# Kernel tuning notes

Hardware: AMD Instinct MI355X
Metric: run time of the kernel (lower is better)

Reference implementation:

```python
import jax, jax.numpy as jnp
import numpy as np

N_NODES = 100000
N_EDGES = 3200000
N_GRAPHS = 1024


def _glorot(key, shape):
    fan_in, fan_out = shape[0], shape[1]
    lim = jnp.sqrt(6.0 / (fan_in + fan_out))
    return jax.random.uniform(key, shape, minval=-lim, maxval=lim, dtype=jnp.float32)


def setup_inputs() -> dict:
    key = jax.random.key(0)
    ks = jax.random.split(key, 9)
    x = jax.random.normal(ks[0], (N_NODES, 3), dtype=jnp.float32)
    edge_index = jax.random.randint(ks[1], (2, N_EDGES), 0, N_NODES, dtype=jnp.int64)
    batch = jnp.sort(jax.random.randint(ks[2], (N_NODES,), 0, N_GRAPHS, dtype=jnp.int64))
    return {
        "x": x,
        "edge_index": edge_index,
        "batch": batch,
        "W1": _glorot(ks[3], (3, 16)),
        "b1": jnp.zeros((16,), jnp.float32),
        "W2": _glorot(ks[4], (16, 16)),
        "b2": jnp.zeros((16,), jnp.float32),
        "Wl": _glorot(ks[5], (16, 7)),
        "bl": jnp.zeros((7,), jnp.float32),
    }


def gcn_conv(x, edge_index, W, b, num_nodes):
    """GCNConv with normalize=True, add_self_loops=True (PyG defaults)."""
    x = x @ W  # linear transform first: [N, F_out]
    loop = jnp.arange(num_nodes, dtype=edge_index.dtype)
    row = jnp.concatenate([edge_index[0], loop])  # source nodes
    col = jnp.concatenate([edge_index[1], loop])  # target nodes
    # degree of target nodes (edge weight 1 incl. self loops)
    deg = jax.ops.segment_sum(jnp.ones_like(col, dtype=x.dtype), col,
                              num_segments=num_nodes)
    dinv = jnp.where(deg > 0, jax.lax.rsqrt(deg), 0.0)
    norm = dinv[row] * dinv[col]  # [E+N]
    msg = x[row] * norm[:, None]  # gather + normalize
    out = jax.ops.segment_sum(msg, col, num_segments=num_nodes)  # scatter-add
    return out + b


def reference(x, edge_index, batch, W1, b1, W2, b2, Wl, bl):
    h = jax.nn.relu(gcn_conv(x, edge_index, W1, b1, N_NODES))
    h = gcn_conv(h, edge_index, W2, b2, N_NODES)
    pooled = jax.ops.segment_sum(h, batch, num_segments=N_GRAPHS)  # global_add_pool
    logits = pooled @ Wl + bl  # [G, 7]
    return jax.nn.log_softmax(logits, axis=1)
```

## Files before the change

kernel.cpp:

```cpp
#include <hip/hip_runtime.h>
#include <hip/hip_fp16.h>
#include <math.h>

#define N_NODES  100000
#define N_EDGES  3200000
#define N_GRAPHS 1024
#define NBUCK    782
#define CAP      4608
#define NPS      500
#define ECH      6400

__device__ inline unsigned pack2(float a, float b) {
    union { __half2 h; unsigned u; } c;
    c.h = __floats2half2_rn(a, b);
    return c.u;
}
__device__ inline float2 up2(unsigned u) {
    union { unsigned u; __half2 h; } c; c.u = u;
    return __half22float2(c.h);
}
__device__ inline void acc8(float* a, uint4 v) {
    float2 f;
    f = up2(v.x); a[0] += f.x; a[1] += f.y;
    f = up2(v.y); a[2] += f.x; a[3] += f.y;
    f = up2(v.z); a[4] += f.x; a[5] += f.y;
    f = up2(v.w); a[6] += f.x; a[7] += f.y;
}
__device__ inline void acc4(float* a, uint2 v) {
    float2 f;
    f = up2(v.x); a[0] += f.x; a[1] += f.y;
    f = up2(v.y); a[2] += f.x; a[3] += f.y;
}

__global__ void k_pair_scatter(const int* __restrict__ row, const int* __restrict__ col,
                               int* __restrict__ gcursor, int* __restrict__ pairbuf) {
    __shared__ int            sbuf[ECH];
    __shared__ unsigned short sbk[ECH];
    __shared__ int            lhist[NBUCK];
    __shared__ int            lcur[NBUCK];
    int t = threadIdx.x;
    int e0 = blockIdx.x * ECH;
    const int4* col4 = (const int4*)(col + e0);
    const int4* row4 = (const int4*)(row + e0);
    for (int j = t; j < NBUCK; j += 256) lhist[j] = 0;
    __syncthreads();
    for (int k = t; k < ECH / 4; k += 256) {
        int4 c = col4[k];
        atomicAdd(&lhist[c.x >> 7], 1);
        atomicAdd(&lhist[c.y >> 7], 1);
        atomicAdd(&lhist[c.z >> 7], 1);
        atomicAdd(&lhist[c.w >> 7], 1);
    }
    __syncthreads();
    if (t < 64) {
        int carry = 0;
        for (int c0 = 0; c0 < NBUCK; c0 += 64) {
            int idx = c0 + t;
            int v = (idx < NBUCK) ? lhist[idx] : 0;
            int orig = v;
#pragma unroll
            for (int o = 1; o < 64; o <<= 1) {
                int u = __shfl_up(v, o, 64);
                if (t >= o) v += u;
            }
            if (idx < NBUCK) lcur[idx] = v - orig + carry;
            carry += __shfl(v, 63, 64);
        }
    }
    __syncthreads();
    for (int j = t; j < NBUCK; j += 256) {
        int c = lhist[j];
        int g = c ? atomicAdd(&gcursor[j], c) : 0;
        lhist[j] = j * CAP + g - lcur[j];
    }
    __syncthreads();
    for (int k = t; k < ECH / 4; k += 256) {
        int4 c = col4[k];
        int4 r = row4[k];
        int bk, pos;
        bk = c.x >> 7; pos = atomicAdd(&lcur[bk], 1);
        sbuf[pos] = r.x | ((c.x & 127) << 17); sbk[pos] = (unsigned short)bk;
        bk = c.y >> 7; pos = atomicAdd(&lcur[bk], 1);
        sbuf[pos] = r.y | ((c.y & 127) << 17); sbk[pos] = (unsigned short)bk;
        bk = c.z >> 7; pos = atomicAdd(&lcur[bk], 1);
        sbuf[pos] = r.z | ((c.z & 127) << 17); sbk[pos] = (unsigned short)bk;
        bk = c.w >> 7; pos = atomicAdd(&lcur[bk], 1);
        sbuf[pos] = r.w | ((c.w & 127) << 17); sbk[pos] = (unsigned short)bk;
    }
    __syncthreads();
    for (int k4 = t; k4 < ECH / 4; k4 += 256) {
        int k = k4 << 2;
        int4 v = ((const int4*)sbuf)[k4];
        ushort4 bb = ((const ushort4*)sbk)[k4];
        int p0 = lhist[bb.x] + k;
        int p1 = lhist[bb.y] + k + 1;
        int p2 = lhist[bb.z] + k + 2;
        int p3 = lhist[bb.w] + k + 3;
        if (p0 < (bb.x + 1) * CAP) pairbuf[p0] = v.x;
        if (p1 < (bb.y + 1) * CAP) pairbuf[p1] = v.y;
        if (p2 < (bb.z + 1) * CAP) pairbuf[p2] = v.z;
        if (p3 < (bb.w + 1) * CAP) pairbuf[p3] = v.w;
    }
}

__global__ void k_finalize(int* __restrict__ pairbuf, const int* __restrict__ gcursor,
                           int2* __restrict__ rowse, float* __restrict__ dinv,
                           const float* __restrict__ x, const float* __restrict__ W1,
                           __half* __restrict__ bufA16) {
    __shared__ int slice[CAP];
    __shared__ int lcnt[128];
    __shared__ int ls[128];
    __shared__ int cur[128];
    __shared__ float sw1[48];
    int t = threadIdx.x, b = blockIdx.x;
    int base = b * CAP;
    int cnt_b = gcursor[b];
    if (cnt_b > CAP) cnt_b = CAP;
    int cnt4 = cnt_b >> 2;
    if (t < 128) lcnt[t] = 0;
    if (t < 48) sw1[t] = W1[t];
    {
        const int4* pb4 = (const int4*)(pairbuf + base);
        for (int k4 = t; k4 < cnt4; k4 += 256) ((int4*)slice)[k4] = pb4[k4];
        int k = (cnt4 << 2) + t;
        if (k < cnt_b) slice[k] = pairbuf[base + k];
    }
    __syncthreads();
    for (int k4 = t; k4 < cnt4; k4 += 256) {
        int4 v = ((const int4*)slice)[k4];
        atomicAdd(&lcnt[(v.x >> 17) & 127], 1);
        atomicAdd(&lcnt[(v.y >> 17) & 127], 1);
        atomicAdd(&lcnt[(v.z >> 17) & 127], 1);
        atomicAdd(&lcnt[(v.w >> 17) & 127], 1);
    }
    {
        int k = (cnt4 << 2) + t;
        if (k < cnt_b) atomicAdd(&lcnt[(slice[k] >> 17) & 127], 1);
    }
    __syncthreads();
    int myc = (t < 128) ? lcnt[t] : 0;
    if (t < 128) ls[t] = myc;
    __syncthreads();
    for (int o = 1; o < 128; o <<= 1) {
        int v = (t < 128 && t >= o) ? ls[t - o] : 0;
        __syncthreads();
        if (t < 128) ls[t] += v;
        __syncthreads();
    }
    int node = (b << 7) + t;
    if (t < 128) {
        int st = base + ls[t] - myc;
        cur[t] = st;
        if (node < N_NODES) {
            rowse[node] = make_int2(st, st + myc);
            float d = rsqrtf((float)(myc + 1));
            dinv[node] = d;
            float x0 = x[node * 3 + 0], x1 = x[node * 3 + 1], x2 = x[node * 3 + 2];
            float v[16];
#pragma unroll
            for (int j = 0; j < 16; j++)
                v[j] = (x0 * sw1[j] + x1 * sw1[16 + j] + x2 * sw1[32 + j]) * d;
            uint4 u0 = { pack2(v[0], v[1]), pack2(v[2], v[3]), pack2(v[4], v[5]), pack2(v[6], v[7]) };
            uint4 u1 = { pack2(v[8], v[9]), pack2(v[10], v[11]), pack2(v[12], v[13]), pack2(v[14], v[15]) };
            uint4* p = (uint4*)(bufA16 + (long long)node * 16);
            p[0] = u0; p[1] = u1;
        }
    }
    __syncthreads();
    for (int k4 = t; k4 < cnt4; k4 += 256) {
        int4 v = ((const int4*)slice)[k4];
        int pos;
        pos = atomicAdd(&cur[(v.x >> 17) & 127], 1); pairbuf[pos] = v.x & 0x1FFFF;
        pos = atomicAdd(&cur[(v.y >> 17) & 127], 1); pairbuf[pos] = v.y & 0x1FFFF;
        pos = atomicAdd(&cur[(v.z >> 17) & 127], 1); pairbuf[pos] = v.z & 0x1FFFF;
        pos = atomicAdd(&cur[(v.w >> 17) & 127], 1); pairbuf[pos] = v.w & 0x1FFFF;
    }
    {
        int k = (cnt4 << 2) + t;
        if (k < cnt_b) {
            int p = slice[k];
            int pos = atomicAdd(&cur[(p >> 17) & 127], 1);
            pairbuf[pos] = p & 0x1FFFF;
        }
    }
}

__global__ void k_gather1(const uint4* __restrict__ src16, const int* __restrict__ csr,
                          const int2* __restrict__ rowse, const float* __restrict__ dinv,
                          const float* __restrict__ b1, const float* __restrict__ W2,
                          __half* __restrict__ out16) {
    __shared__ float sh[64][17];
    __shared__ float sW[256];
    __shared__ float sb1[16];
    int t = threadIdx.x;
    sW[t] = W2[t]; sW[t + 128] = W2[t + 128];
    if (t < 16) sb1[t] = b1[t];
    int local = t >> 1, h = t & 1;
    int node = blockIdx.x * 64 + local;
    bool act = node < N_NODES;
    int2 se = act ? rowse[node] : make_int2(0, 0);
    int s = se.x, e = se.y;
    float acc[8] = {0, 0, 0, 0, 0, 0, 0, 0};
    if (act) {
        uint4 u = src16[node * 2 + h];
        float2 f;
        f = up2(u.x); acc[0] = f.x; acc[1] = f.y;
        f = up2(u.y); acc[2] = f.x; acc[3] = f.y;
        f = up2(u.z); acc[4] = f.x; acc[5] = f.y;
        f = up2(u.w); acc[6] = f.x; acc[7] = f.y;
    }
    int j = s;
    for (; j < e && (j & 3); j++) acc8(acc, src16[csr[j] * 2 + h]);
    for (; j + 8 <= e; j += 8) {
        int4 ia = *(const int4*)(csr + j);
        int4 ib = *(const int4*)(csr + j + 4);
        uint4 v0 = src16[ia.x * 2 + h], v1 = src16[ia.y * 2 + h];
        uint4 v2 = src16[ia.z * 2 + h], v3 = src16[ia.w * 2 + h];
        uint4 v4 = src16[ib.x * 2 + h], v5 = src16[ib.y * 2 + h];
        uint4 v6 = src16[ib.z * 2 + h], v7 = src16[ib.w * 2 + h];
        acc8(acc, v0); acc8(acc, v1); acc8(acc, v2); acc8(acc, v3);
        acc8(acc, v4); acc8(acc, v5); acc8(acc, v6); acc8(acc, v7);
    }
    for (; j < e; j++) acc8(acc, src16[csr[j] * 2 + h]);
    float d = act ? dinv[node] : 0.f;
#pragma unroll
    for (int k = 0; k < 8; k++) {
        float v = acc[k] * d + sb1[h * 8 + k];
        sh[local][h * 8 + k] = v > 0.f ? v : 0.f;
    }
    __syncthreads();
    float v[8];
#pragma unroll
    for (int jj = 0; jj < 8; jj++) {
        int jo = h * 8 + jj;
        float a = 0.f;
#pragma unroll
        for (int k = 0; k < 16; k++) a += sh[local][k] * sW[k * 16 + jo];
        v[jj] = a * d;
    }
    if (act) {
        uint4 u = { pack2(v[0], v[1]), pack2(v[2], v[3]), pack2(v[4], v[5]), pack2(v[6], v[7]) };
        ((uint4*)(out16 + (long long)node * 16 + h * 8))[0] = u;
    }
}

__global__ void k_gather2(const uint2* __restrict__ src16, const int* __restrict__ csr,
                          const int2* __restrict__ rowse, const float* __restrict__ dinv,
                          const int* __restrict__ batch, float* __restrict__ pooled) {
    __shared__ float pl[8][16];
    __shared__ int ginfo[2];
    int t = threadIdx.x;
    int node0 = blockIdx.x * 64;
    if (t < 128) pl[t >> 4][t & 15] = 0.f;
    if (t == 0) {
        int last = node0 + 63; if (last >= N_NODES) last = N_NODES - 1;
        ginfo[0] = batch[node0];
        ginfo[1] = batch[last];
    }
    __syncthreads();
    int node = node0 + (t >> 2);
    int h = t & 3;
    float o[4] = {0, 0, 0, 0};
    bool act = node < N_NODES;
    if (act) {
        int2 se = rowse[node];
        int s = se.x, e = se.y;
        uint2 u = src16[node * 4 + h];
        float2 f;
        f = up2(u.x); o[0] = f.x; o[1] = f.y;
        f = up2(u.y); o[2] = f.x; o[3] = f.y;
        int j = s;
        for (; j < e && (j & 3); j++) acc4(o, src16[csr[j] * 4 + h]);
        for (; j + 8 <= e; j += 8) {
            int4 ia = *(const int4*)(csr + j);
            int4 ib = *(const int4*)(csr + j + 4);
            uint2 v0 = src16[ia.x * 4 + h], v1 = src16[ia.y * 4 + h];
            uint2 v2 = src16[ia.z * 4 + h], v3 = src16[ia.w * 4 + h];
            uint2 v4 = src16[ib.x * 4 + h], v5 = src16[ib.y * 4 + h];
            uint2 v6 = src16[ib.z * 4 + h], v7 = src16[ib.w * 4 + h];
            acc4(o, v0); acc4(o, v1); acc4(o, v2); acc4(o, v3);
            acc4(o, v4); acc4(o, v5); acc4(o, v6); acc4(o, v7);
        }
        for (; j < e; j++) acc4(o, src16[csr[j] * 4 + h]);
        float d = dinv[node];
        o[0] *= d; o[1] *= d; o[2] *= d; o[3] *= d;
        int slot = batch[node] - ginfo[0];
        if (slot < 8) {
#pragma unroll
            for (int k = 0; k < 4; k++) atomicAdd(&pl[slot][h * 4 + k], o[k]);
        } else {
#pragma unroll
            for (int k = 0; k < 4; k++) atomicAdd(&pooled[batch[node] * 16 + h * 4 + k], o[k]);
        }
    }
    __syncthreads();
    if (t < 128) {
        int s = t >> 4, f = t & 15;
        int span = ginfo[1] - ginfo[0];
        if (s <= span && s < 8)
            atomicAdd(&pooled[(ginfo[0] + s) * 16 + f], pl[s][f]);
    }
}

__global__ void k_head(const float* __restrict__ pooled, const int* __restrict__ batch,
                       const float* __restrict__ b2, const float* __restrict__ Wl,
                       const float* __restrict__ bl, float* __restrict__ out) {
    int g = blockIdx.x;
    int t = threadIdx.x;
    __shared__ int range[2];
    __shared__ float pld[16];
    __shared__ float logits[7];
    if (t < 2) {
        int target = g + t;
        int lo = 0, hi = N_NODES;
        while (lo < hi) {
            int mid = (lo + hi) >> 1;
            if (batch[mid] < target) lo = mid + 1; else hi = mid;
        }
        range[t] = lo;
    }
    __syncthreads();
    float cnt = (float)(range[1] - range[0]);
    if (t < 16) pld[t] = pooled[g * 16 + t] + cnt * b2[t];
    __syncthreads();
    if (t < 7) {
        float a = bl[t];
#pragma unroll
        for (int k = 0; k < 16; k++) a += pld[k] * Wl[k * 7 + t];
        logits[t] = a;
    }
    __syncthreads();
    if (t == 0) {
        float m = logits[0];
#pragma unroll
        for (int c = 1; c < 7; c++) m = fmaxf(m, logits[c]);
        float sum = 0.f;
#pragma unroll
        for (int c = 0; c < 7; c++) sum += expf(logits[c] - m);
        float lse = logf(sum) + m;
#pragma unroll
        for (int c = 0; c < 7; c++) out[g * 7 + c] = logits[c] - lse;
    }
}

extern "C" void kernel_launch(void* const* d_in, const int* in_sizes, int n_in,
                              void* d_out, int out_size, void* d_ws, size_t ws_size,
                              hipStream_t stream) {
    const float* x     = (const float*)d_in[0];
    const int*   ei    = (const int*)d_in[1];
    const int*   batch = (const int*)d_in[2];
    const float* W1    = (const float*)d_in[3];
    const float* b1    = (const float*)d_in[4];
    const float* W2    = (const float*)d_in[5];
    const float* b2    = (const float*)d_in[6];
    const float* Wl    = (const float*)d_in[7];
    const float* bl    = (const float*)d_in[8];
    float* out = (float*)d_out;

    const int* row = ei;
    const int* col = ei + N_EDGES;

    int*    gcursor = (int*)d_ws;
    float*  pooled  = (float*)d_ws + 800;
    float*  dinv    = (float*)d_ws + 17200;
    int2*   rowse   = (int2*)((int*)d_ws + 117200);
    int*    pairbuf = (int*)d_ws + 317200;
    __half* bufA16  = (__half*)((int*)d_ws + 3920656);
    __half* bufB16  = (__half*)((int*)d_ws + 4720656);

    const int BT = 256;

    hipMemsetAsync(gcursor, 0, 17184 * sizeof(int), stream);
    k_pair_scatter<<<NPS, BT, 0, stream>>>(row, col, gcursor, pairbuf);
    k_finalize<<<NBUCK, BT, 0, stream>>>(pairbuf, gcursor, rowse, dinv, x, W1, bufA16);
    k_gather1<<<(N_NODES + 63) / 64, 128, 0, stream>>>((const uint4*)bufA16, pairbuf, rowse,
                                                       dinv, b1, W2, bufB16);
    k_gather2<<<(N_NODES + 63) / 64, BT, 0, stream>>>((const uint2*)bufB16, pairbuf, rowse,
                                                      dinv, batch, pooled);
    k_head<<<N_GRAPHS, 64, 0, stream>>>(pooled, batch, b2, Wl, bl, out);
}
```

Measured before the change: 201.3 us.

## Aggregate raw 3-dim inputs before W1 in first GCN layer

```diff
diff --git a/kernel.cpp b/kernel.cpp
--- a/kernel.cpp
+++ b/kernel.cpp
@@ -18,13 +18,6 @@
 __device__ inline float2 up2(unsigned u) {
     union { unsigned u; __half2 h; } c; c.u = u;
     return __half22float2(c.h);
-}
-__device__ inline void acc8(float* a, uint4 v) {
-    float2 f;
-    f = up2(v.x); a[0] += f.x; a[1] += f.y;
-    f = up2(v.y); a[2] += f.x; a[3] += f.y;
-    f = up2(v.z); a[4] += f.x; a[5] += f.y;
-    f = up2(v.w); a[6] += f.x; a[7] += f.y;
 }
 __device__ inline void acc4(float* a, uint2 v) {
     float2 f;
@@ -105,20 +98,17 @@
 
 __global__ void k_finalize(int* __restrict__ pairbuf, const int* __restrict__ gcursor,
                            int2* __restrict__ rowse, float* __restrict__ dinv,
-                           const float* __restrict__ x, const float* __restrict__ W1,
-                           __half* __restrict__ bufA16) {
+                           const float* __restrict__ x, __half* __restrict__ bufA16) {
     __shared__ int slice[CAP];
     __shared__ int lcnt[128];
     __shared__ int ls[128];
     __shared__ int cur[128];
-    __shared__ float sw1[48];
     int t = threadIdx.x, b = blockIdx.x;
     int base = b * CAP;
     int cnt_b = gcursor[b];
     if (cnt_b > CAP) cnt_b = CAP;
     int cnt4 = cnt_b >> 2;
     if (t < 128) lcnt[t] = 0;
-    if (t < 48) sw1[t] = W1[t];
     {
         const int4* pb4 = (const int4*)(pairbuf + base);
         for (int k4 = t; k4 < cnt4; k4 += 256) ((int4*)slice)[k4] = pb4[k4];
@@ -156,14 +146,8 @@
             float d = rsqrtf((float)(myc + 1));
             dinv[node] = d;
             float x0 = x[node * 3 + 0], x1 = x[node * 3 + 1], x2 = x[node * 3 + 2];
-            float v[16];
-#pragma unroll
-            for (int j = 0; j < 16; j++)
-                v[j] = (x0 * sw1[j] + x1 * sw1[16 + j] + x2 * sw1[32 + j]) * d;
-            uint4 u0 = { pack2(v[0], v[1]), pack2(v[2], v[3]), pack2(v[4], v[5]), pack2(v[6], v[7]) };
-            uint4 u1 = { pack2(v[8], v[9]), pack2(v[10], v[11]), pack2(v[12], v[13]), pack2(v[14], v[15]) };
-            uint4* p = (uint4*)(bufA16 + (long long)node * 16);
-            p[0] = u0; p[1] = u1;
+            uint2 u = { pack2(x0 * d, x1 * d), pack2(x2 * d, 0.f) };
+            ((uint2*)(bufA16 + (long long)node * 4))[0] = u;
         }
     }
     __syncthreads();
@@ -185,63 +169,60 @@
     }
 }
 
-__global__ void k_gather1(const uint4* __restrict__ src16, const int* __restrict__ csr,
+__global__ void k_gather1(const uint2* __restrict__ src16, const int* __restrict__ csr,
                           const int2* __restrict__ rowse, const float* __restrict__ dinv,
-                          const float* __restrict__ b1, const float* __restrict__ W2,
-                          __half* __restrict__ out16) {
-    __shared__ float sh[64][17];
-    __shared__ float sW[256];
+                          const float* __restrict__ W1, const float* __restrict__ b1,
+                          const float* __restrict__ W2, __half* __restrict__ out16) {
+    __shared__ float sW1[48];
     __shared__ float sb1[16];
+    __shared__ float sW2[256];
     int t = threadIdx.x;
-    sW[t] = W2[t]; sW[t + 128] = W2[t + 128];
+    sW2[t] = W2[t];
+    if (t < 48) sW1[t] = W1[t];
     if (t < 16) sb1[t] = b1[t];
-    int local = t >> 1, h = t & 1;
-    int node = blockIdx.x * 64 + local;
-    bool act = node < N_NODES;
-    int2 se = act ? rowse[node] : make_int2(0, 0);
+    __syncthreads();
+    int node = blockIdx.x * 256 + t;
+    if (node >= N_NODES) return;
+    int2 se = rowse[node];
     int s = se.x, e = se.y;
-    float acc[8] = {0, 0, 0, 0, 0, 0, 0, 0};
-    if (act) {
-        uint4 u = src16[node * 2 + h];
+    float p[4];
+    {
+        uint2 u = src16[node];
         float2 f;
-        f = up2(u.x); acc[0] = f.x; acc[1] = f.y;
-        f = up2(u.y); acc[2] = f.x; acc[3] = f.y;
-        f = up2(u.z); acc[4] = f.x; acc[5] = f.y;
-        f = up2(u.w); acc[6] = f.x; acc[7] = f.y;
+        f = up2(u.x); p[0] = f.x; p[1] = f.y;
+        f = up2(u.y); p[2] = f.x; p[3] = f.y;
     }
     int j = s;
-    for (; j < e && (j & 3); j++) acc8(acc, src16[csr[j] * 2 + h]);
+    for (; j < e && (j & 3); j++) acc4(p, src16[csr[j]]);
     for (; j + 8 <= e; j += 8) {
         int4 ia = *(const int4*)(csr + j);
         int4 ib = *(const int4*)(csr + j + 4);
-        uint4 v0 = src16[ia.x * 2 + h], v1 = src16[ia.y * 2 + h];
-        uint4 v2 = src16[ia.z * 2 + h], v3 = src16[ia.w * 2 + h];
-        uint4 v4 = src16[ib.x * 2 + h], v5 = src16[ib.y * 2 + h];
-        uint4 v6 = src16[ib.z * 2 + h], v7 = src16[ib.w * 2 + h];
-        acc8(acc, v0); acc8(acc, v1); acc8(acc, v2); acc8(acc, v3);
-        acc8(acc, v4); acc8(acc, v5); acc8(acc, v6); acc8(acc, v7);
-    }
-    for (; j < e; j++) acc8(acc, src16[csr[j] * 2 + h]);
-    float d = act ? dinv[node] : 0.f;
-#pragma unroll
-    for (int k = 0; k < 8; k++) {
-        float v = acc[k] * d + sb1[h * 8 + k];
-        sh[local][h * 8 + k] = v > 0.f ? v : 0.f;
-    }
-    __syncthreads();
-    float v[8];
-#pragma unroll
-    for (int jj = 0; jj < 8; jj++) {
-        int jo = h * 8 + jj;
+        uint2 v0 = src16[ia.x], v1 = src16[ia.y], v2 = src16[ia.z], v3 = src16[ia.w];
+        uint2 v4 = src16[ib.x], v5 = src16[ib.y], v6 = src16[ib.z], v7 = src16[ib.w];
+        acc4(p, v0); acc4(p, v1); acc4(p, v2); acc4(p, v3);
+        acc4(p, v4); acc4(p, v5); acc4(p, v6); acc4(p, v7);
+    }
+    for (; j < e; j++) acc4(p, src16[csr[j]]);
+    float d = dinv[node];
+    float q0 = p[0] * d, q1 = p[1] * d, q2 = p[2] * d;
+    float h[16];
+#pragma unroll
+    for (int k = 0; k < 16; k++) {
+        float v = q0 * sW1[k] + q1 * sW1[16 + k] + q2 * sW1[32 + k] + sb1[k];
+        h[k] = v > 0.f ? v : 0.f;
+    }
+    float v[16];
+#pragma unroll
+    for (int jj = 0; jj < 16; jj++) {
         float a = 0.f;
 #pragma unroll
-        for (int k = 0; k < 16; k++) a += sh[local][k] * sW[k * 16 + jo];
+        for (int k = 0; k < 16; k++) a += h[k] * sW2[k * 16 + jj];
         v[jj] = a * d;
     }
-    if (act) {
-        uint4 u = { pack2(v[0], v[1]), pack2(v[2], v[3]), pack2(v[4], v[5]), pack2(v[6], v[7]) };
-        ((uint4*)(out16 + (long long)node * 16 + h * 8))[0] = u;
-    }
+    uint4 u0 = { pack2(v[0], v[1]), pack2(v[2], v[3]), pack2(v[4], v[5]), pack2(v[6], v[7]) };
+    uint4 u1 = { pack2(v[8], v[9]), pack2(v[10], v[11]), pack2(v[12], v[13]), pack2(v[14], v[15]) };
+    uint4* op = (uint4*)(out16 + (long long)node * 16);
+    op[0] = u0; op[1] = u1;
 }
 
 __global__ void k_gather2(const uint2* __restrict__ src16, const int* __restrict__ csr,
@@ -366,15 +347,15 @@
     int2*   rowse   = (int2*)((int*)d_ws + 117200);
     int*    pairbuf = (int*)d_ws + 317200;
     __half* bufA16  = (__half*)((int*)d_ws + 3920656);
-    __half* bufB16  = (__half*)((int*)d_ws + 4720656);
+    __half* bufB16  = (__half*)((int*)d_ws + 4120656);
 
     const int BT = 256;
 
     hipMemsetAsync(gcursor, 0, 17184 * sizeof(int), stream);
     k_pair_scatter<<<NPS, BT, 0, stream>>>(row, col, gcursor, pairbuf);
-    k_finalize<<<NBUCK, BT, 0, stream>>>(pairbuf, gcursor, rowse, dinv, x, W1, bufA16);
-    k_gather1<<<(N_NODES + 63) / 64, 128, 0, stream>>>((const uint4*)bufA16, pairbuf, rowse,
-                                                       dinv, b1, W2, bufB16);
+    k_finalize<<<NBUCK, BT, 0, stream>>>(pairbuf, gcursor, rowse, dinv, x, bufA16);
+    k_gather1<<<(N_NODES + 255) / 256, BT, 0, stream>>>((const uint2*)bufA16, pairbuf, rowse,
+                                                        dinv, W1, b1, W2, bufB16);
     k_gather2<<<(N_NODES + 63) / 64, BT, 0, stream>>>((const uint2*)bufB16, pairbuf, rowse,
                                                       dinv, batch, pooled);
     k_head<<<N_GRAPHS, 64, 0, stream>>>(pooled, batch, b2, Wl, bl, out);
```

Result: faster. 197.3 us (-2.0%).
